# Kernel optimization log

Hardware: AMD Instinct MI355X
Metric: run time of the kernel (lower is better)

Reference implementation:

```python
import jax, jax.numpy as jnp
import numpy as np

SIGMA = 0.05
KSIZE = 3
MIN_VAL = 50.0
MAX_VAL = 100.0


def _gauss_kernel():
    # ax = range(-(3//2)+1, 3//2+1) = [-1, 0, 1]  (matches TF int-floor-div)
    ax = jnp.arange(-(KSIZE // 2) + 1.0, KSIZE // 2 + 1.0)
    xx, yy = jnp.meshgrid(ax, ax)
    k = jnp.exp(-(xx ** 2 + yy ** 2) / (2.0 * SIGMA ** 2))
    k = k / jnp.sum(k)
    return k[..., None, None].astype(jnp.float32)  # HWIO, C=1


def _reflect_pad(x):
    return jnp.pad(x, ((0, 0), (1, 1), (1, 1), (0, 0)), mode='reflect')


def _conv(x, k):
    return jax.lax.conv_general_dilated(x, k, (1, 1), 'VALID',
                                        dimension_numbers=('NHWC', 'HWIO', 'NHWC'))


def _canny(images):
    blur = _conv(_reflect_pad(images), _gauss_kernel())
    h = jnp.array([[-1, 0, 1], [-2, 0, 2], [-1, 0, 1]], jnp.float32)[..., None, None]
    v = jnp.array([[-1, -2, -1], [0, 0, 0], [1, 2, 1]], jnp.float32)[..., None, None]
    bp = _reflect_pad(blur)
    gx = _conv(bp, h)
    gy = _conv(bp, v)
    gxy = jnp.sqrt(gx ** 2 + gy ** 2)
    # NOTE: original uses atan2(gx, gy) in this arg order
    theta = (jnp.arctan2(gx, gy) * (180.0 / np.pi) + 90.0) % 180.0

    H, W = gx.shape[1], gx.shape[2]
    # dilation2d with a -inf/0 kernel == max over the kernel's zero-offsets of the
    # zero-padded image; offsets are (dy,dx) of the 0 entries of each 3x3 filter.
    offsets = [
        [(1, 0), (1, 1), (1, 2)],  # horizontal bin: middle row
        [(0, 2), (1, 1), (2, 0)],  # 45 deg: anti-diagonal
        [(0, 1), (1, 1), (2, 1)],  # vertical bin: middle column
        [(0, 0), (1, 1), (2, 2)],  # 135 deg: main diagonal
    ]
    conds = [
        jnp.logical_or(theta >= 157.5, theta < 22.5),
        jnp.logical_and(theta >= 22.5, theta < 67.5),
        jnp.logical_and(theta >= 67.5, theta < 112.5),
        jnp.logical_and(theta >= 112.5, theta < 157.5),
    ]

    edge = jnp.zeros_like(gxy)
    for cond, offs in zip(conds, offsets):
        ang = jnp.where(cond, gxy, 0.0)
        pad = jnp.pad(ang, ((0, 0), (1, 1), (1, 1), (0, 0)))  # zero pad, as ZeroPadding2D
        mp = pad[:, offs[0][0]:offs[0][0] + H, offs[0][1]:offs[0][1] + W, :]
        for dy, dx in offs[1:]:
            mp = jnp.maximum(mp, pad[:, dy:dy + H, dx:dx + W, :])
        edge = edge + jnp.where(mp == ang, ang, 0.0)

    edge_sure = jnp.where(edge >= MAX_VAL, 255.0, 0.0)
    edge_week = jnp.where(jnp.logical_and(edge >= MIN_VAL, edge < MAX_VAL), 255.0, 0.0)
    edge_image = jnp.where(jnp.logical_or(edge_week == 255.0, edge_sure == 255.0), 255.5, 0.0)
    return edge_image, edge_week, edge_sure


def setup_inputs() -> dict:
    key = jax.random.key(0)
    images = jax.random.uniform(key, (16, 1024, 1024, 1), dtype=jnp.float32) * 255.0
    return {"images": images}


def reference(images):
    return _canny(images)
```

## Files before the change

### kernel.cpp

```cpp
#include <hip/hip_runtime.h>
#include <math.h>

#define IMG_H 1024
#define IMG_W 1024
#define OUT_H 1025
#define OUT_W 1025
#define NIMG  16
#define TOTAL (NIMG * OUT_H * OUT_W)

#define TILE_W 64
#define TILE_H 16
#define HALO_W 68
#define HALO_H 18
#define NQX    17
#define NQUAD  (HALO_H * NQX)
#define NTHREADS 320

__device__ __forceinline__ int refl(int k) {
    if (k >= 2) return (k <= 1025) ? (k - 2) : 1022;
    return k;
}

__device__ __forceinline__ void sobel_generic(const float* __restrict__ img, int i, int j,
                                              float& gx, float& gy) {
    int r0 = refl(i), r1 = refl(i + 1), r2 = refl(i + 2);
    int c0 = refl(j), c1 = refl(j + 1), c2 = refl(j + 2);
    const float* p0 = img + r0 * IMG_W;
    const float* p1 = img + r1 * IMG_W;
    const float* p2 = img + r2 * IMG_W;
    float v00 = p0[c0], v01 = p0[c1], v02 = p0[c2];
    float v10 = p1[c0],               v12 = p1[c2];
    float v20 = p2[c0], v21 = p2[c1], v22 = p2[c2];

    float t = -v00;
    t = __fadd_rn(t, v02);
    t = __fadd_rn(t, -2.0f * v10);
    t = __fadd_rn(t, 2.0f * v12);
    t = __fadd_rn(t, -v20);
    gx = __fadd_rn(t, v22);

    t = -v00;
    t = __fadd_rn(t, -2.0f * v01);
    t = __fadd_rn(t, -v02);
    t = __fadd_rn(t, v20);
    t = __fadd_rn(t, 2.0f * v21);
    gy = __fadd_rn(t, v22);
}

__device__ int classify_slow(float gx, float gy) {
    float t = (float)atan2((double)gx, (double)gy);
    float deg = __fmul_rn(t, (float)(180.0 / M_PI));
    float th = __fadd_rn(deg, 90.0f);
    th = fmodf(th, 180.0f);
    if (th < 0.0f) th += 180.0f;
    if (th < 22.5f || th >= 157.5f) return 0;
    if (th < 67.5f) return 1;
    if (th < 112.5f) return 2;
    return 3;
}

__device__ __forceinline__ int classify(float gx, float gy) {
    float ax = fabsf(gx), ay = fabsf(gy);
    const float T22_LO = 0.414172141e0f;
    const float T22_HI = 0.414254984e0f;
    const float T67_LO = 2.413972141e0f;
    const float T67_HI = 2.414454984e0f;

    if (ax <= ay * T22_LO) return 2;
    if (ax >= ay * T67_HI) return 0;
    if (ax >= ay * T22_HI && ax <= ay * T67_LO) {
        unsigned s = (__float_as_uint(gx) ^ __float_as_uint(gy)) >> 31;
        return s ? 1 : 3;
    }
    return classify_slow(gx, gy);
}

__device__ __forceinline__ float mag(float gx, float gy) {
    return __fsqrt_rn(__fadd_rn(__fmul_rn(gx, gx), __fmul_rn(gy, gy)));
}

__device__ __forceinline__ void load6(const float* __restrict__ p, float v[6]) {
    float4 a = *(const float4*)p;
    float2 b = *(const float2*)(p + 4);
    v[0] = a.x; v[1] = a.y; v[2] = a.z; v[3] = a.w; v[4] = b.x; v[5] = b.y;
}

__global__ __launch_bounds__(NTHREADS, 8) void canny_kernel(const float* __restrict__ images,
                                                            float* __restrict__ out) {
    __shared__ float    g_s[HALO_H * HALO_W];
    __shared__ unsigned b_u[HALO_H * NQX];

    const int tile_ox = blockIdx.x * TILE_W;
    const int tile_oy = blockIdx.y * TILE_H;
    const int n       = blockIdx.z;
    const float* img = images + (size_t)n * IMG_H * IMG_W;
    const int t = threadIdx.x;

    if (t < NQUAD) {
        int hy  = t / NQX;
        int qx  = t - hy * NQX;
        int oy  = tile_oy + hy - 1;
        int ox0 = tile_ox + qx * 4 - 2;

        float    gxs[4], gys[4];
        float    gq[4];
        unsigned bq[4];

        if (oy >= 2 && oy <= 1023 && ox0 >= 2 && ox0 <= 1020) {
            const float* r0p = img + (oy - 2) * IMG_W + (ox0 - 2);
            float R0[6], R1[6], R2[6];
            load6(r0p, R0);
            load6(r0p + IMG_W, R1);
            load6(r0p + 2 * IMG_W, R2);
            #pragma unroll
            for (int p = 0; p < 4; p++) {
                float v00 = R0[p], v01 = R0[p + 1], v02 = R0[p + 2];
                float v10 = R1[p],                  v12 = R1[p + 2];
                float v20 = R2[p], v21 = R2[p + 1], v22 = R2[p + 2];

                float s = -v00;
                s = __fadd_rn(s, v02);
                s = __fadd_rn(s, -2.0f * v10);
                s = __fadd_rn(s, 2.0f * v12);
                s = __fadd_rn(s, -v20);
                float gx = __fadd_rn(s, v22);

                s = -v00;
                s = __fadd_rn(s, -2.0f * v01);
                s = __fadd_rn(s, -v02);
                s = __fadd_rn(s, v20);
                s = __fadd_rn(s, 2.0f * v21);
                float gy = __fadd_rn(s, v22);

                gxs[p] = gx;
                gys[p] = gy;
                gq[p]  = mag(gx, gy);
            }
        } else {
            #pragma unroll
            for (int p = 0; p < 4; p++) {
                int ox = ox0 + p;
                if (oy >= 0 && oy < OUT_H && ox >= 0 && ox < OUT_W) {
                    float gx, gy;
                    sobel_generic(img, oy, ox, gx, gy);
                    gxs[p] = gx;
                    gys[p] = gy;
                    gq[p]  = mag(gx, gy);
                } else {
                    gxs[p] = 0.0f;
                    gys[p] = 1.0f;
                    gq[p]  = -1.0f;
                }
            }
        }

        #pragma unroll
        for (int p = 0; p < 4; p++) {
            bq[p] = (gq[p] < 0.0f) ? 255u : (unsigned)classify(gxs[p], gys[p]);
        }

        int ldoff = hy * HALO_W + qx * 4;
        *(float4*)&g_s[ldoff] = make_float4(gq[0], gq[1], gq[2], gq[3]);
        b_u[hy * NQX + qx] = bq[0] | (bq[1] << 8) | (bq[2] << 16) | (bq[3] << 24);
    }
    __syncthreads();

    const unsigned char* b_s = (const unsigned char*)b_u;
    #pragma unroll
    for (int q = 0; q < 4; q++) {
        int p = t + NTHREADS * q;
        if (p >= TILE_W * TILE_H) break;
        int r = p >> 6, c = p & 63;
        int oy = tile_oy + r, ox = tile_ox + c;
        if (oy >= OUT_H || ox >= OUT_W) continue;

        int hc = (r + 1) * HALO_W + (c + 2);
        float gc = g_s[hc];
        int   bc = b_s[hc];

        int doff = (bc == 0) ? 1
                 : (bc == 1) ? (HALO_W - 1)
                 : (bc == 2) ? HALO_W
                 :             (HALO_W + 1);

        float nmax = 0.0f;
        float g1 = g_s[hc + doff];
        if (b_s[hc + doff] == bc && g1 > nmax) nmax = g1;
        float g2 = g_s[hc - doff];
        if (b_s[hc - doff] == bc && g2 > nmax) nmax = g2;

        float e = (gc >= nmax) ? gc : 0.0f;

        size_t o = (size_t)(n * OUT_H + oy) * OUT_W + ox;
        out[o]                       = (e >= 50.0f) ? 255.5f : 0.0f;
        out[(size_t)TOTAL + o]       = (e >= 50.0f && e < 100.0f) ? 255.0f : 0.0f;
        out[(size_t)(2 * TOTAL) + o] = (e >= 100.0f) ? 255.0f : 0.0f;
    }
}

extern "C" void kernel_launch(void* const* d_in, const int* in_sizes, int n_in,
                              void* d_out, int out_size, void* d_ws, size_t ws_size,
                              hipStream_t stream) {
    const float* images = (const float*)d_in[0];
    float* out = (float*)d_out;
    dim3 grid((OUT_W + TILE_W - 1) / TILE_W,
              (OUT_H + TILE_H - 1) / TILE_H,
              NIMG);
    canny_kernel<<<grid, NTHREADS, 0, stream>>>(images, out);
}
```

Before: 303.0 us.

## Process five row tiles per block with register prefetch and double-buffered LDS

Each block now loops over five consecutive vertical tiles instead of one. It prefetches the next tile's input rows into registers while computing the current tile, and double-buffers the shared gradient and bin arrays so only one barrier per tile is needed. The aim is to hide global load latency and amortise block launch overhead. In exchange the grid shrinks (13 y-blocks), which reduces parallelism, the extra registers and dropped occupancy hint may lower waves per SIMD, and halo rows are still recomputed per tile.

After: 425.1 us. 40.3% more time.

```diff
diff --git a/kernel.cpp b/kernel.cpp
--- a/kernel.cpp
+++ b/kernel.cpp
@@ -15,6 +15,8 @@
 #define NQX    17
 #define NQUAD  (HALO_H * NQX)
 #define NTHREADS 320
+#define YTILES 5
+#define GRID_Y 13
 
 __device__ __forceinline__ int refl(int k) {
     if (k >= 2) return (k <= 1025) ? (k - 2) : 1022;
@@ -85,116 +87,152 @@
     v[0] = a.x; v[1] = a.y; v[2] = a.z; v[3] = a.w; v[4] = b.x; v[5] = b.y;
 }
 
-__global__ __launch_bounds__(NTHREADS, 8) void canny_kernel(const float* __restrict__ images,
-                                                            float* __restrict__ out) {
-    __shared__ float    g_s[HALO_H * HALO_W];
-    __shared__ unsigned b_u[HALO_H * NQX];
+__global__ __launch_bounds__(NTHREADS) void canny_kernel(const float* __restrict__ images,
+                                                         float* __restrict__ out) {
+    __shared__ float    g_s[2][HALO_H * HALO_W];
+    __shared__ unsigned b_u[2][HALO_H * NQX];
 
     const int tile_ox = blockIdx.x * TILE_W;
-    const int tile_oy = blockIdx.y * TILE_H;
+    const int ty0     = blockIdx.y * YTILES;
     const int n       = blockIdx.z;
     const float* img = images + (size_t)n * IMG_H * IMG_W;
     const int t = threadIdx.x;
 
-    if (t < NQUAD) {
-        int hy  = t / NQX;
-        int qx  = t - hy * NQX;
-        int oy  = tile_oy + hy - 1;
-        int ox0 = tile_ox + qx * 4 - 2;
-
-        float    gxs[4], gys[4];
-        float    gq[4];
-        unsigned bq[4];
-
-        if (oy >= 2 && oy <= 1023 && ox0 >= 2 && ox0 <= 1020) {
+    const bool worker = (t < NQUAD);
+    int hy = 0, qx = 0, ox0 = 0;
+    if (worker) {
+        hy  = t / NQX;
+        qx  = t - hy * NQX;
+        ox0 = tile_ox + qx * 4 - 2;
+    }
+    const bool xin = (ox0 >= 2 && ox0 <= 1020);
+
+    float cur[3][6], nxt[3][6];
+
+    if (worker) {
+        int oy = ty0 * TILE_H + hy - 1;
+        if (oy >= 2 && oy <= 1023 && xin) {
             const float* r0p = img + (oy - 2) * IMG_W + (ox0 - 2);
-            float R0[6], R1[6], R2[6];
-            load6(r0p, R0);
-            load6(r0p + IMG_W, R1);
-            load6(r0p + 2 * IMG_W, R2);
-            #pragma unroll
-            for (int p = 0; p < 4; p++) {
-                float v00 = R0[p], v01 = R0[p + 1], v02 = R0[p + 2];
-                float v10 = R1[p],                  v12 = R1[p + 2];
-                float v20 = R2[p], v21 = R2[p + 1], v22 = R2[p + 2];
-
-                float s = -v00;
-                s = __fadd_rn(s, v02);
-                s = __fadd_rn(s, -2.0f * v10);
-                s = __fadd_rn(s, 2.0f * v12);
-                s = __fadd_rn(s, -v20);
-                float gx = __fadd_rn(s, v22);
-
-                s = -v00;
-                s = __fadd_rn(s, -2.0f * v01);
-                s = __fadd_rn(s, -v02);
-                s = __fadd_rn(s, v20);
-                s = __fadd_rn(s, 2.0f * v21);
-                float gy = __fadd_rn(s, v22);
-
-                gxs[p] = gx;
-                gys[p] = gy;
-                gq[p]  = mag(gx, gy);
+            load6(r0p,             cur[0]);
+            load6(r0p + IMG_W,     cur[1]);
+            load6(r0p + 2 * IMG_W, cur[2]);
+        }
+    }
+
+    #pragma unroll 1
+    for (int s = 0; s < YTILES; s++) {
+        const int tile_oy = (ty0 + s) * TILE_H;
+        const int buf = s & 1;
+
+        if (worker && s + 1 < YTILES) {
+            int oyn = tile_oy + TILE_H + hy - 1;
+            if (oyn >= 2 && oyn <= 1023 && xin) {
+                const float* r0p = img + (oyn - 2) * IMG_W + (ox0 - 2);
+                load6(r0p,             nxt[0]);
+                load6(r0p + IMG_W,     nxt[1]);
+                load6(r0p + 2 * IMG_W, nxt[2]);
             }
-        } else {
-            #pragma unroll
-            for (int p = 0; p < 4; p++) {
-                int ox = ox0 + p;
-                if (oy >= 0 && oy < OUT_H && ox >= 0 && ox < OUT_W) {
-                    float gx, gy;
-                    sobel_generic(img, oy, ox, gx, gy);
+        }
+
+        if (worker) {
+            int oy = tile_oy + hy - 1;
+            float    gxs[4], gys[4], gq[4];
+            unsigned bq[4];
+
+            if (oy >= 2 && oy <= 1023 && xin) {
+                #pragma unroll
+                for (int p = 0; p < 4; p++) {
+                    float v00 = cur[0][p], v01 = cur[0][p + 1], v02 = cur[0][p + 2];
+                    float v10 = cur[1][p],                      v12 = cur[1][p + 2];
+                    float v20 = cur[2][p], v21 = cur[2][p + 1], v22 = cur[2][p + 2];
+
+                    float sx = -v00;
+                    sx = __fadd_rn(sx, v02);
+                    sx = __fadd_rn(sx, -2.0f * v10);
+                    sx = __fadd_rn(sx, 2.0f * v12);
+                    sx = __fadd_rn(sx, -v20);
+                    float gx = __fadd_rn(sx, v22);
+
+                    sx = -v00;
+                    sx = __fadd_rn(sx, -2.0f * v01);
+                    sx = __fadd_rn(sx, -v02);
+                    sx = __fadd_rn(sx, v20);
+                    sx = __fadd_rn(sx, 2.0f * v21);
+                    float gy = __fadd_rn(sx, v22);
+
                     gxs[p] = gx;
                     gys[p] = gy;
                     gq[p]  = mag(gx, gy);
-                } else {
-                    gxs[p] = 0.0f;
-                    gys[p] = 1.0f;
-                    gq[p]  = -1.0f;
+                }
+            } else {
+                #pragma unroll
+                for (int p = 0; p < 4; p++) {
+                    int ox = ox0 + p;
+                    if (oy >= 0 && oy < OUT_H && ox >= 0 && ox < OUT_W) {
+                        float gx, gy;
+                        sobel_generic(img, oy, ox, gx, gy);
+                        gxs[p] = gx;
+                        gys[p] = gy;
+                        gq[p]  = mag(gx, gy);
+                    } else {
+                        gxs[p] = 0.0f;
+                        gys[p] = 1.0f;
+                        gq[p]  = -1.0f;
+                    }
                 }
             }
-        }
-
+
+            #pragma unroll
+            for (int p = 0; p < 4; p++) {
+                bq[p] = (gq[p] < 0.0f) ? 255u : (unsigned)classify(gxs[p], gys[p]);
+            }
+
+            int ldoff = hy * HALO_W + qx * 4;
+            *(float4*)&g_s[buf][ldoff] = make_float4(gq[0], gq[1], gq[2], gq[3]);
+            b_u[buf][hy * NQX + qx] = bq[0] | (bq[1] << 8) | (bq[2] << 16) | (bq[3] << 24);
+        }
+        __syncthreads();
+
+        const float*         gs  = g_s[buf];
+        const unsigned char* b_s = (const unsigned char*)b_u[buf];
         #pragma unroll
-        for (int p = 0; p < 4; p++) {
-            bq[p] = (gq[p] < 0.0f) ? 255u : (unsigned)classify(gxs[p], gys[p]);
-        }
-
-        int ldoff = hy * HALO_W + qx * 4;
-        *(float4*)&g_s[ldoff] = make_float4(gq[0], gq[1], gq[2], gq[3]);
-        b_u[hy * NQX + qx] = bq[0] | (bq[1] << 8) | (bq[2] << 16) | (bq[3] << 24);
-    }
-    __syncthreads();
-
-    const unsigned char* b_s = (const unsigned char*)b_u;
-    #pragma unroll
-    for (int q = 0; q < 4; q++) {
-        int p = t + NTHREADS * q;
-        if (p >= TILE_W * TILE_H) break;
-        int r = p >> 6, c = p & 63;
-        int oy = tile_oy + r, ox = tile_ox + c;
-        if (oy >= OUT_H || ox >= OUT_W) continue;
-
-        int hc = (r + 1) * HALO_W + (c + 2);
-        float gc = g_s[hc];
-        int   bc = b_s[hc];
-
-        int doff = (bc == 0) ? 1
-                 : (bc == 1) ? (HALO_W - 1)
-                 : (bc == 2) ? HALO_W
-                 :             (HALO_W + 1);
-
-        float nmax = 0.0f;
-        float g1 = g_s[hc + doff];
-        if (b_s[hc + doff] == bc && g1 > nmax) nmax = g1;
-        float g2 = g_s[hc - doff];
-        if (b_s[hc - doff] == bc && g2 > nmax) nmax = g2;
-
-        float e = (gc >= nmax) ? gc : 0.0f;
-
-        size_t o = (size_t)(n * OUT_H + oy) * OUT_W + ox;
-        out[o]                       = (e >= 50.0f) ? 255.5f : 0.0f;
-        out[(size_t)TOTAL + o]       = (e >= 50.0f && e < 100.0f) ? 255.0f : 0.0f;
-        out[(size_t)(2 * TOTAL) + o] = (e >= 100.0f) ? 255.0f : 0.0f;
+        for (int q = 0; q < 4; q++) {
+            int p = t + NTHREADS * q;
+            if (p >= TILE_W * TILE_H) break;
+            int r = p >> 6, c = p & 63;
+            int oy = tile_oy + r, ox = tile_ox + c;
+            if (oy >= OUT_H || ox >= OUT_W) continue;
+
+            int hc = (r + 1) * HALO_W + (c + 2);
+            float gc = gs[hc];
+            int   bc = b_s[hc];
+
+            int doff = (bc == 0) ? 1
+                     : (bc == 1) ? (HALO_W - 1)
+                     : (bc == 2) ? HALO_W
+                     :             (HALO_W + 1);
+
+            float nmax = 0.0f;
+            float g1 = gs[hc + doff];
+            if (b_s[hc + doff] == bc && g1 > nmax) nmax = g1;
+            float g2 = gs[hc - doff];
+            if (b_s[hc - doff] == bc && g2 > nmax) nmax = g2;
+
+            float e = (gc >= nmax) ? gc : 0.0f;
+
+            size_t o = (size_t)(n * OUT_H + oy) * OUT_W + ox;
+            out[o]                       = (e >= 50.0f) ? 255.5f : 0.0f;
+            out[(size_t)TOTAL + o]       = (e >= 50.0f && e < 100.0f) ? 255.0f : 0.0f;
+            out[(size_t)(2 * TOTAL) + o] = (e >= 100.0f) ? 255.0f : 0.0f;
+        }
+
+        if (worker && s + 1 < YTILES) {
+            #pragma unroll
+            for (int r = 0; r < 3; r++)
+                #pragma unroll
+                for (int c = 0; c < 6; c++)
+                    cur[r][c] = nxt[r][c];
+        }
     }
 }
 
@@ -204,7 +242,7 @@
     const float* images = (const float*)d_in[0];
     float* out = (float*)d_out;
     dim3 grid((OUT_W + TILE_W - 1) / TILE_W,
-              (OUT_H + TILE_H - 1) / TILE_H,
+              GRID_Y,
               NIMG);
     canny_kernel<<<grid, NTHREADS, 0, stream>>>(images, out);
 }
```

## Vectorize aligned output stores and pad shared gradient stride

Applied to the files above, without the earlier changes.

Full-width tiles now have 256 threads each handle four consecutive pixels, shifted so that the three output planes can be written with aligned float4 stores. A leftover thread per row writes the unaligned head and tail pixels with scalar stores. The shared gradient array uses a padded stride of 69 to change the bank pattern, which means its writes become scalar. The slow atan2 fallback is marked noinline and the occupancy hint is dropped from launch bounds, which could change register allocation.

New measurement: 319.8 us. 5.5% more time.

```diff
diff --git a/kernel.cpp b/kernel.cpp
--- a/kernel.cpp
+++ b/kernel.cpp
@@ -11,6 +11,7 @@
 #define TILE_W 64
 #define TILE_H 16
 #define HALO_W 68
+#define GSTR   69
 #define HALO_H 18
 #define NQX    17
 #define NQUAD  (HALO_H * NQX)
@@ -47,7 +48,7 @@
     gy = __fadd_rn(t, v22);
 }
 
-__device__ int classify_slow(float gx, float gy) {
+__device__ __attribute__((noinline)) int classify_slow(float gx, float gy) {
     float t = (float)atan2((double)gx, (double)gy);
     float deg = __fmul_rn(t, (float)(180.0 / M_PI));
     float th = __fadd_rn(deg, 90.0f);
@@ -85,9 +86,28 @@
     v[0] = a.x; v[1] = a.y; v[2] = a.z; v[3] = a.w; v[4] = b.x; v[5] = b.y;
 }
 
-__global__ __launch_bounds__(NTHREADS, 8) void canny_kernel(const float* __restrict__ images,
-                                                            float* __restrict__ out) {
-    __shared__ float    g_s[HALO_H * HALO_W];
+__device__ __forceinline__ float nms_px(const float* __restrict__ g_s,
+                                        const unsigned char* __restrict__ b_s,
+                                        int r, int c) {
+    int hg = (r + 1) * GSTR   + (c + 2);
+    int hb = (r + 1) * HALO_W + (c + 2);
+    float gc = g_s[hg];
+    int   bc = b_s[hb];
+    int dy = (bc == 0) ? 0 : 1;
+    int dx = (bc == 1) ? -1 : ((bc == 2) ? 0 : 1);
+    int og = dy * GSTR   + dx;
+    int ob = dy * HALO_W + dx;
+    float nmax = 0.0f;
+    float g1 = g_s[hg + og];
+    if (b_s[hb + ob] == bc && g1 > nmax) nmax = g1;
+    float g2 = g_s[hg - og];
+    if (b_s[hb - ob] == bc && g2 > nmax) nmax = g2;
+    return (gc >= nmax) ? gc : 0.0f;
+}
+
+__global__ __launch_bounds__(NTHREADS) void canny_kernel(const float* __restrict__ images,
+                                                         float* __restrict__ out) {
+    __shared__ float    g_s[HALO_H * GSTR];
     __shared__ unsigned b_u[HALO_H * NQX];
 
     const int tile_ox = blockIdx.x * TILE_W;
@@ -102,12 +122,11 @@
         int oy  = tile_oy + hy - 1;
         int ox0 = tile_ox + qx * 4 - 2;
 
-        float    gxs[4], gys[4];
-        float    gq[4];
+        float    gxs[4], gys[4], gq[4];
         unsigned bq[4];
 
         if (oy >= 2 && oy <= 1023 && ox0 >= 2 && ox0 <= 1020) {
-            const float* r0p = img + (oy - 2) * IMG_W + (ox0 - 2);
+            const float* r0p = img + (size_t)(oy - 2) * IMG_W + (ox0 - 2);
             float R0[6], R1[6], R2[6];
             load6(r0p, R0);
             load6(r0p + IMG_W, R1);
@@ -132,8 +151,7 @@
                 s = __fadd_rn(s, 2.0f * v21);
                 float gy = __fadd_rn(s, v22);
 
-                gxs[p] = gx;
-                gys[p] = gy;
+                gxs[p] = gx; gys[p] = gy;
                 gq[p]  = mag(gx, gy);
             }
         } else {
@@ -143,12 +161,10 @@
                 if (oy >= 0 && oy < OUT_H && ox >= 0 && ox < OUT_W) {
                     float gx, gy;
                     sobel_generic(img, oy, ox, gx, gy);
-                    gxs[p] = gx;
-                    gys[p] = gy;
+                    gxs[p] = gx; gys[p] = gy;
                     gq[p]  = mag(gx, gy);
                 } else {
-                    gxs[p] = 0.0f;
-                    gys[p] = 1.0f;
+                    gxs[p] = 0.0f; gys[p] = 1.0f;
                     gq[p]  = -1.0f;
                 }
             }
@@ -159,42 +175,76 @@
             bq[p] = (gq[p] < 0.0f) ? 255u : (unsigned)classify(gxs[p], gys[p]);
         }
 
-        int ldoff = hy * HALO_W + qx * 4;
-        *(float4*)&g_s[ldoff] = make_float4(gq[0], gq[1], gq[2], gq[3]);
+        int goff = hy * GSTR + qx * 4;
+        g_s[goff + 0] = gq[0];
+        g_s[goff + 1] = gq[1];
+        g_s[goff + 2] = gq[2];
+        g_s[goff + 3] = gq[3];
         b_u[hy * NQX + qx] = bq[0] | (bq[1] << 8) | (bq[2] << 16) | (bq[3] << 24);
     }
     __syncthreads();
 
     const unsigned char* b_s = (const unsigned char*)b_u;
-    #pragma unroll
-    for (int q = 0; q < 4; q++) {
-        int p = t + NTHREADS * q;
-        if (p >= TILE_W * TILE_H) break;
-        int r = p >> 6, c = p & 63;
-        int oy = tile_oy + r, ox = tile_ox + c;
-        if (oy >= OUT_H || ox >= OUT_W) continue;
-
-        int hc = (r + 1) * HALO_W + (c + 2);
-        float gc = g_s[hc];
-        int   bc = b_s[hc];
-
-        int doff = (bc == 0) ? 1
-                 : (bc == 1) ? (HALO_W - 1)
-                 : (bc == 2) ? HALO_W
-                 :             (HALO_W + 1);
-
-        float nmax = 0.0f;
-        float g1 = g_s[hc + doff];
-        if (b_s[hc + doff] == bc && g1 > nmax) nmax = g1;
-        float g2 = g_s[hc - doff];
-        if (b_s[hc - doff] == bc && g2 > nmax) nmax = g2;
-
-        float e = (gc >= nmax) ? gc : 0.0f;
-
-        size_t o = (size_t)(n * OUT_H + oy) * OUT_W + ox;
-        out[o]                       = (e >= 50.0f) ? 255.5f : 0.0f;
-        out[(size_t)TOTAL + o]       = (e >= 50.0f && e < 100.0f) ? 255.0f : 0.0f;
-        out[(size_t)(2 * TOTAL) + o] = (e >= 100.0f) ? 255.0f : 0.0f;
+
+    if (tile_ox + TILE_W <= OUT_W) {
+        if (t < 256) {
+            int r  = t >> 4;
+            int k  = t & 15;
+            int oy = tile_oy + r;
+            if (oy < OUT_H) {
+                size_t rowbase = (size_t)(n * OUT_H + oy) * OUT_W + tile_ox;
+                int a = (int)((4u - ((unsigned)rowbase & 3u)) & 3u);
+                if (k < 15) {
+                    int c0 = a + 4 * k;
+                    float e0 = nms_px(g_s, b_s, r, c0);
+                    float e1 = nms_px(g_s, b_s, r, c0 + 1);
+                    float e2 = nms_px(g_s, b_s, r, c0 + 2);
+                    float e3 = nms_px(g_s, b_s, r, c0 + 3);
+
+                    float4 P0 = make_float4(e0 >= 50.0f ? 255.5f : 0.0f,
+                                            e1 >= 50.0f ? 255.5f : 0.0f,
+                                            e2 >= 50.0f ? 255.5f : 0.0f,
+                                            e3 >= 50.0f ? 255.5f : 0.0f);
+                    float4 P1 = make_float4((e0 >= 50.0f && e0 < 100.0f) ? 255.0f : 0.0f,
+                                            (e1 >= 50.0f && e1 < 100.0f) ? 255.0f : 0.0f,
+                                            (e2 >= 50.0f && e2 < 100.0f) ? 255.0f : 0.0f,
+                                            (e3 >= 50.0f && e3 < 100.0f) ? 255.0f : 0.0f);
+                    float4 P2 = make_float4(e0 >= 100.0f ? 255.0f : 0.0f,
+                                            e1 >= 100.0f ? 255.0f : 0.0f,
+                                            e2 >= 100.0f ? 255.0f : 0.0f,
+                                            e3 >= 100.0f ? 255.0f : 0.0f);
+
+                    size_t o = rowbase + c0;
+                    *(float4*)(out + o)                   = P0;
+                    *(float4*)(out + (size_t)TOTAL + o)   = P1;
+                    *(float4*)(out + (size_t)(2 * TOTAL) + o) = P2;
+                } else {
+                    #pragma unroll
+                    for (int j = 0; j < 4; j++) {
+                        int c = (j < a) ? j : (60 + j);
+                        float e = nms_px(g_s, b_s, r, c);
+                        size_t o = rowbase + c;
+                        out[o]                       = (e >= 50.0f) ? 255.5f : 0.0f;
+                        out[(size_t)TOTAL + o]       = (e >= 50.0f && e < 100.0f) ? 255.0f : 0.0f;
+                        out[(size_t)(2 * TOTAL) + o] = (e >= 100.0f) ? 255.0f : 0.0f;
+                    }
+                }
+            }
+        }
+    } else {
+        #pragma unroll
+        for (int q = 0; q < 4; q++) {
+            int p = t + NTHREADS * q;
+            if (p >= TILE_W * TILE_H) break;
+            int r = p >> 6, c = p & 63;
+            int oy = tile_oy + r, ox = tile_ox + c;
+            if (oy >= OUT_H || ox >= OUT_W) continue;
+            float e = nms_px(g_s, b_s, r, c);
+            size_t o = (size_t)(n * OUT_H + oy) * OUT_W + ox;
+            out[o]                       = (e >= 50.0f) ? 255.5f : 0.0f;
+            out[(size_t)TOTAL + o]       = (e >= 50.0f && e < 100.0f) ? 255.0f : 0.0f;
+            out[(size_t)(2 * TOTAL) + o] = (e >= 100.0f) ? 255.0f : 0.0f;
+        }
     }
 }
 
@@ -202,9 +252,9 @@
                               void* d_out, int out_size, void* d_ws, size_t ws_size,
                               hipStream_t stream) {
     const float* images = (const float*)d_in[0];
-    float* out = (float*)d_out;
+    float* outp = (float*)d_out;
     dim3 grid((OUT_W + TILE_W - 1) / TILE_W,
               (OUT_H + TILE_H - 1) / TILE_H,
               NIMG);
-    canny_kernel<<<grid, NTHREADS, 0, stream>>>(images, out);
-}
+    canny_kernel<<<grid, NTHREADS, 0, stream>>>(images, outp);
+}
```
